# Kernel optimization log

Measured on AMD Instinct MI355X. Metric: run time of the kernel, lower is better.

The kernel has to match this reference:

```python
import jax, jax.numpy as jnp
import numpy as np

DIM = 1024
NHEAD = 16
HEAD_DIM = DIM // NHEAD
B, S, L = 1, 4096, 4096


def setup_inputs() -> dict:
    key = jax.random.key(0)
    ks = jax.random.split(key, 11)
    scale = 1.0 / np.sqrt(DIM)
    inp = {
        'query': jax.random.normal(ks[0], (B, S, DIM), dtype=jnp.float32),
        'key': jax.random.normal(ks[1], (B, L, DIM), dtype=jnp.float32),
        'value': jax.random.normal(ks[2], (B, L, DIM), dtype=jnp.float32),
        # torch nn.Linear weights: y = x @ W.T + b, W shape (out, in) = (DIM, DIM)
        'Wq': jax.random.normal(ks[3], (DIM, DIM), dtype=jnp.float32) * scale,
        'bq': jax.random.normal(ks[4], (DIM,), dtype=jnp.float32) * 0.01,
        'Wk': jax.random.normal(ks[5], (DIM, DIM), dtype=jnp.float32) * scale,
        'bk': jax.random.normal(ks[6], (DIM,), dtype=jnp.float32) * 0.01,
        'Wv': jax.random.normal(ks[7], (DIM, DIM), dtype=jnp.float32) * scale,
        'bv': jax.random.normal(ks[8], (DIM,), dtype=jnp.float32) * 0.01,
        'Wo': jax.random.normal(ks[9], (DIM, DIM), dtype=jnp.float32) * scale,
        'bo': jax.random.normal(ks[10], (DIM,), dtype=jnp.float32) * 0.01,
    }
    return inp


def _split_heads(x):
    # (B, T, D) -> (B, H, T, hd)
    b, t, _ = x.shape
    return x.reshape(b, t, NHEAD, HEAD_DIM).transpose(0, 2, 1, 3)


def reference(query, key, value, Wq, bq, Wk, bk, Wv, bv, Wo, bo):
    q = _split_heads(query @ Wq.T + bq)   # (B,H,S,hd)
    k = _split_heads(key @ Wk.T + bk)     # (B,H,L,hd)
    v = _split_heads(value @ Wv.T + bv)   # (B,H,L,hd)
    inv_sqrt_d = 1.0 / np.sqrt(HEAD_DIM).astype(np.float32)
    scores = jnp.einsum('bhsd,bhld->bhsl', q, k) * inv_sqrt_d
    probs = jax.nn.softmax(scores, axis=-1)
    ctx = jnp.einsum('bhsl,bhld->bhsd', probs, v)
    ctx = ctx.transpose(0, 2, 1, 3).reshape(query.shape[0], -1, DIM)
    return ctx @ Wo.T + bo
```

## Files before the change

kernel.cpp:

```cpp
#include <hip/hip_runtime.h>
#include <hip/hip_bf16.h>

#define DIM 1024
#define NHEAD 16
#define HD 64
#define SEQ 4096

typedef unsigned short u16;
typedef unsigned int u32;
typedef __attribute__((ext_vector_type(8))) short bf16x8;
typedef __attribute__((ext_vector_type(4))) float f32x4;
typedef __attribute__((ext_vector_type(16))) float f32x16;

__device__ __forceinline__ u16 f2bf(float x) {
  __hip_bfloat16 h = __float2bfloat16(x);
  return *reinterpret_cast<u16*>(&h);
}

__device__ __forceinline__ float bf2f(u16 u) {
  union { u32 u; float f; } c;
  c.u = ((u32)u) << 16;
  return c.f;
}

__device__ __forceinline__ float fexp2(float x) {
#if __has_builtin(__builtin_amdgcn_exp2f)
  return __builtin_amdgcn_exp2f(x);
#else
  return __expf(x * 0.69314718056f);
#endif
}

__device__ __forceinline__ u32 cvtpk(float a, float b) {
  u32 r;
  asm("v_cvt_pk_bf16_f32 %0, %1, %2" : "=v"(r) : "v"(a), "v"(b));
  return r;
}

__device__ __forceinline__ void pswap(u32& a, u32& b) {
  asm("v_permlane32_swap_b32 %0, %1" : "+v"(a), "+v"(b));
}

__device__ __forceinline__ void gload16(const u16* g, const u16* l) {
  __builtin_amdgcn_global_load_lds(
      (const __attribute__((address_space(1))) void*)g,
      (__attribute__((address_space(3))) void*)l, 16, 0, 0);
}

__global__ __launch_bounds__(256) void cvt_all(
    const float* __restrict__ q, const float* __restrict__ k, const float* __restrict__ v,
    const float* __restrict__ wq, const float* __restrict__ wk, const float* __restrict__ wv,
    const float* __restrict__ wo,
    u16* __restrict__ oq, u16* __restrict__ ok, u16* __restrict__ ov,
    u16* __restrict__ owq, u16* __restrict__ owk, u16* __restrict__ owv, u16* __restrict__ owo) {
  int b = blockIdx.x;
  const float* in;
  u16* out;
  int i;
  if (b < 12288) {
    int s = b >> 12;
    in = (s == 0) ? q : (s == 1) ? k : v;
    out = (s == 0) ? oq : (s == 1) ? ok : ov;
    i = (b & 4095) * 256 + threadIdx.x;
  } else {
    int bb = b - 12288;
    int s = bb >> 10;
    in = (s == 0) ? wq : (s == 1) ? wk : (s == 2) ? wv : wo;
    out = (s == 0) ? owq : (s == 1) ? owk : (s == 2) ? owv : owo;
    i = (bb & 1023) * 256 + threadIdx.x;
  }
  float4 val = ((const float4*)in)[i];
  ushort4 o;
  o.x = f2bf(val.x); o.y = f2bf(val.y); o.z = f2bf(val.z); o.w = f2bf(val.w);
  ((ushort4*)out)[i] = o;
}

__global__ __launch_bounds__(256, 3) void gemm_proj(
    const u16* __restrict__ qx, const u16* __restrict__ kx, const u16* __restrict__ vx,
    const u16* __restrict__ wqp, const u16* __restrict__ wkp, const u16* __restrict__ wvp,
    const float* __restrict__ bq, const float* __restrict__ bk, const float* __restrict__ bv,
    u16* __restrict__ Qb, u16* __restrict__ Kb, u16* __restrict__ Vt) {
  __shared__ u16 As[128][64];
  __shared__ u16 Bs[128][64];
  const int z = blockIdx.y;
  const u16 *Ag, *Bg;
  const float* bias;
  u16* outp;
  int mb, nb;
  float scale = 1.f;
  if (z == 0) {
    Ag = qx; Bg = wqp; bias = bq; outp = Qb;
    mb = blockIdx.x >> 3; nb = blockIdx.x & 7; scale = 0.18033688f;
  } else if (z == 1) {
    Ag = kx; Bg = wkp; bias = bk; outp = Kb;
    mb = blockIdx.x >> 3; nb = blockIdx.x & 7;
  } else {
    Ag = wvp; Bg = vx; bias = bv; outp = Vt;
    mb = blockIdx.x >> 5; nb = blockIdx.x & 31;
  }

  const int tid = threadIdx.x, lane = tid & 63, wid = tid >> 6;
  const int lq = lane & 15, g = lane >> 4;
  const int wr = wid >> 1, wc = wid & 1;
  const int m0 = mb * 128, n0 = nb * 128;
  const int sr = lane >> 3, ss = lane & 7;

  const u16* pA = Ag + (size_t)(m0 + wid * 32 + sr) * DIM + ((ss ^ sr) * 8);
  const u16* pB = Bg + (size_t)(n0 + wid * 32 + sr) * DIM + ((ss ^ sr) * 8);

  const f32x4 zero4 = {0.f, 0.f, 0.f, 0.f};
  f32x4 acc[4][4];
#pragma unroll
  for (int mi = 0; mi < 4; ++mi)
#pragma unroll
    for (int ni = 0; ni < 4; ++ni) acc[mi][ni] = zero4;

  for (int k0 = 0; k0 < DIM; k0 += 64) {
    __syncthreads();
#pragma unroll
    for (int i = 0; i < 4; ++i) {
      gload16(pA + i * 8 * DIM + k0, &As[wid * 32 + i * 8][0]);
      gload16(pB + i * 8 * DIM + k0, &Bs[wid * 32 + i * 8][0]);
    }
    __syncthreads();
#pragma unroll
    for (int kk = 0; kk < 2; ++kk) {
      bf16x8 a[4], b[4];
#pragma unroll
      for (int t4 = 0; t4 < 4; ++t4) {
        u32 offA = (u32)(wr * 64 + t4 * 16 + lq) * 128 + (u32)(((kk * 4 + g) ^ (lq & 7)) * 16);
        u32 offB = (u32)(wc * 64 + t4 * 16 + lq) * 128 + (u32)(((kk * 4 + g) ^ (lq & 7)) * 16);
        a[t4] = *(const bf16x8*)((const char*)As + offA);
        b[t4] = *(const bf16x8*)((const char*)Bs + offB);
      }
#pragma unroll
      for (int mi = 0; mi < 4; ++mi)
#pragma unroll
        for (int ni = 0; ni < 4; ++ni)
          acc[mi][ni] = __builtin_amdgcn_mfma_f32_16x16x32_bf16(a[mi], b[ni], acc[mi][ni], 0, 0, 0);
    }
  }

  if (z < 2) {
    float bn[4];
#pragma unroll
    for (int ni = 0; ni < 4; ++ni) bn[ni] = bias[n0 + wc * 64 + ni * 16 + lq];
#pragma unroll
    for (int mi = 0; mi < 4; ++mi)
#pragma unroll
      for (int r = 0; r < 4; ++r) {
        int mm = m0 + wr * 64 + mi * 16 + g * 4 + r;
#pragma unroll
        for (int ni = 0; ni < 4; ++ni) {
          int nn = n0 + wc * 64 + ni * 16 + lq;
          float v = (acc[mi][ni][r] + bn[ni]) * scale;
          outp[((size_t)(nn >> 6) * SEQ + mm) * 64 + (nn & 63)] = f2bf(v);
        }
      }
  } else {
#pragma unroll
    for (int mi = 0; mi < 4; ++mi)
#pragma unroll
      for (int r = 0; r < 4; ++r) {
        int mm = m0 + wr * 64 + mi * 16 + g * 4 + r;
        float bm = bias[mm];
#pragma unroll
        for (int ni = 0; ni < 4; ++ni) {
          int nn = n0 + wc * 64 + ni * 16 + lq;
          outp[(size_t)mm * SEQ + nn] = f2bf(acc[mi][ni][r] + bm);
        }
      }
  }
}

__global__ __launch_bounds__(256) void gemm_out(
    const u16* __restrict__ Ag, const u16* __restrict__ Bg,
    const float* __restrict__ bias, float* __restrict__ outp) {
  __shared__ u16 As[128][64];
  __shared__ u16 Bs[128][64];
  const int tid = threadIdx.x, lane = tid & 63, wid = tid >> 6;
  const int lq = lane & 15, g = lane >> 4;
  const int wr = wid >> 1, wc = wid & 1;
  const int m0 = blockIdx.x * 128, n0 = blockIdx.y * 128;
  const int sr = lane >> 3, ss = lane & 7;

  const u16* pA = Ag + (size_t)(m0 + wid * 32 + sr) * DIM + ((ss ^ sr) * 8);
  const u16* pB = Bg + (size_t)(n0 + wid * 32 + sr) * DIM + ((ss ^ sr) * 8);

  const f32x4 zero4 = {0.f, 0.f, 0.f, 0.f};
  f32x4 acc[4][4];
#pragma unroll
  for (int mi = 0; mi < 4; ++mi)
#pragma unroll
    for (int ni = 0; ni < 4; ++ni) acc[mi][ni] = zero4;

  for (int k0 = 0; k0 < DIM; k0 += 64) {
    __syncthreads();
#pragma unroll
    for (int i = 0; i < 4; ++i) {
      gload16(pA + i * 8 * DIM + k0, &As[wid * 32 + i * 8][0]);
      gload16(pB + i * 8 * DIM + k0, &Bs[wid * 32 + i * 8][0]);
    }
    __syncthreads();
#pragma unroll
    for (int kk = 0; kk < 2; ++kk) {
      bf16x8 a[4], b[4];
#pragma unroll
      for (int t4 = 0; t4 < 4; ++t4) {
        u32 offA = (u32)(wr * 64 + t4 * 16 + lq) * 128 + (u32)(((kk * 4 + g) ^ (lq & 7)) * 16);
        u32 offB = (u32)(wc * 64 + t4 * 16 + lq) * 128 + (u32)(((kk * 4 + g) ^ (lq & 7)) * 16);
        a[t4] = *(const bf16x8*)((const char*)As + offA);
        b[t4] = *(const bf16x8*)((const char*)Bs + offB);
      }
#pragma unroll
      for (int mi = 0; mi < 4; ++mi)
#pragma unroll
        for (int ni = 0; ni < 4; ++ni)
          acc[mi][ni] = __builtin_amdgcn_mfma_f32_16x16x32_bf16(a[mi], b[ni], acc[mi][ni], 0, 0, 0);
    }
  }

  float bn[4];
#pragma unroll
  for (int ni = 0; ni < 4; ++ni) bn[ni] = bias[n0 + wc * 64 + ni * 16 + lq];
#pragma unroll
  for (int mi = 0; mi < 4; ++mi)
#pragma unroll
    for (int r = 0; r < 4; ++r) {
      int mm = m0 + wr * 64 + mi * 16 + g * 4 + r;
#pragma unroll
      for (int ni = 0; ni < 4; ++ni) {
        int nn = n0 + wc * 64 + ni * 16 + lq;
        outp[(size_t)mm * DIM + nn] = acc[mi][ni][r] + bn[ni];
      }
    }
}

__global__ __launch_bounds__(256, 2) void attn32(
    const u16* __restrict__ Qb, const u16* __restrict__ Kb,
    const u16* __restrict__ Vtb, u16* __restrict__ po,
    float* __restrict__ pl) {
  __shared__ u16 Ks[2][64][64];
  __shared__ u16 Vs[2][64][64];
  const int tid = threadIdx.x, lane = tid & 63, wid = tid >> 6;
  const int q5 = lane & 31, hi = lane >> 5;
  const int bid = blockIdx.x;
  const int rest = bid >> 3;
  const int h = (bid & 7) * 2 + (rest >> 6);
  const int kv = (rest >> 5) & 1;
  const int qbase = (rest & 31) * 128 + wid * 32;

  const u16* Qg = Qb + (size_t)h * SEQ * HD;
  const u16* Kg = Kb + (size_t)h * SEQ * HD;
  const u16* Vg = Vtb + (size_t)h * HD * SEQ;

  const int sr = lane >> 3, ss = lane & 7;
  const u16* pK = Kg + (size_t)(kv * 2048 + wid * 16 + sr) * HD + ((ss ^ sr) * 8);
  const u16* pV = Vg + (size_t)(wid * 16 + sr) * SEQ + kv * 2048 + ((ss ^ sr) * 8);

  u32 roff[8];
#pragma unroll
  for (int ks = 0; ks < 4; ++ks) {
    u32 slot = (u32)((ks * 2 + hi) ^ (q5 & 7));
    roff[ks * 2] = (u32)q5 * 128 + slot * 16;
    roff[ks * 2 + 1] = (u32)(32 + q5) * 128 + slot * 16;
  }
  const char* KsB = (const char*)Ks;
  const char* VsB = (const char*)Vs;

  bf16x8 qf[4];
#pragma unroll
  for (int ks = 0; ks < 4; ++ks)
    qf[ks] = *(const bf16x8*)(Qg + (size_t)(qbase + q5) * HD + ks * 16 + hi * 8);

  bf16x8 ones;
#pragma unroll
  for (int j = 0; j < 8; ++j) ones[j] = (short)0x3F80;

  f32x16 o0, o1, osum, zv;
#pragma unroll
  for (int j = 0; j < 16; ++j) { o0[j] = 0.f; o1[j] = 0.f; osum[j] = 0.f; zv[j] = 0.f; }

  gload16(pK, &Ks[0][wid * 16][0]);
  gload16(pK + 8 * HD, &Ks[0][wid * 16 + 8][0]);
  gload16(pV, &Vs[0][wid * 16][0]);
  gload16(pV + 8 * SEQ, &Vs[0][wid * 16 + 8][0]);
  const u16* pKn = pK + 64 * HD;
  const u16* pVn = pV + 64;
  __syncthreads();

  const int NT = 2048 / 64;

#define ATTN_BODY(CB, PF)                                                     \
  {                                                                           \
    if (PF) {                                                                 \
      gload16(pKn, &Ks[(CB) ^ 1][wid * 16][0]);                               \
      gload16(pKn + 8 * HD, &Ks[(CB) ^ 1][wid * 16 + 8][0]);                  \
      gload16(pVn, &Vs[(CB) ^ 1][wid * 16][0]);                               \
      gload16(pVn + 8 * SEQ, &Vs[(CB) ^ 1][wid * 16 + 8][0]);                 \
      pKn += 64 * HD;                                                         \
      pVn += 64;                                                              \
    }                                                                         \
    f32x16 s0, s1;                                                            \
    __builtin_amdgcn_s_setprio(1);                                            \
    {                                                                         \
      bf16x8 ka0 = *(const bf16x8*)(KsB + (CB) * 8192 + roff[0]);             \
      bf16x8 ka1 = *(const bf16x8*)(KsB + (CB) * 8192 + roff[1]);             \
      s0 = __builtin_amdgcn_mfma_f32_32x32x16_bf16(ka0, qf[0], zv, 0, 0, 0);  \
      s1 = __builtin_amdgcn_mfma_f32_32x32x16_bf16(ka1, qf[0], zv, 0, 0, 0);  \
    }                                                                         \
    _Pragma("unroll")                                                         \
    for (int ks = 1; ks < 4; ++ks) {                                          \
      bf16x8 ka0 = *(const bf16x8*)(KsB + (CB) * 8192 + roff[ks * 2]);        \
      bf16x8 ka1 = *(const bf16x8*)(KsB + (CB) * 8192 + roff[ks * 2 + 1]);    \
      s0 = __builtin_amdgcn_mfma_f32_32x32x16_bf16(ka0, qf[ks], s0, 0, 0, 0); \
      s1 = __builtin_amdgcn_mfma_f32_32x32x16_bf16(ka1, qf[ks], s1, 0, 0, 0); \
    }                                                                         \
    __builtin_amdgcn_s_setprio(0);                                            \
    _Pragma("unroll")                                                         \
    for (int j = 0; j < 16; ++j) s0[j] = fexp2(s0[j]);                        \
    _Pragma("unroll")                                                         \
    for (int j = 0; j < 16; ++j) s1[j] = fexp2(s1[j]);                        \
    u32 pk0[8], pk1[8];                                                       \
    _Pragma("unroll")                                                         \
    for (int i2 = 0; i2 < 8; ++i2) {                                          \
      pk0[i2] = cvtpk(s0[2 * i2], s0[2 * i2 + 1]);                            \
      pk1[i2] = cvtpk(s1[2 * i2], s1[2 * i2 + 1]);                            \
    }                                                                         \
    bf16x8 W[4];                                                              \
    _Pragma("unroll")                                                         \
    for (int kss = 0; kss < 2; ++kss) {                                       \
      {                                                                       \
        u32 a = pk0[4 * kss], b = pk0[4 * kss + 2];                           \
        u32 c = pk0[4 * kss + 1], d = pk0[4 * kss + 3];                       \
        pswap(a, b);                                                          \
        pswap(c, d);                                                          \
        union { u32 u[4]; bf16x8 v; } tt;                                     \
        tt.u[0] = a; tt.u[1] = c; tt.u[2] = b; tt.u[3] = d;                   \
        W[kss] = tt.v;                                                        \
      }                                                                       \
      {                                                                       \
        u32 a = pk1[4 * kss], b = pk1[4 * kss + 2];                           \
        u32 c = pk1[4 * kss + 1], d = pk1[4 * kss + 3];                       \
        pswap(a, b);                                                          \
        pswap(c, d);                                                          \
        union { u32 u[4]; bf16x8 v; } tt;                                     \
        tt.u[0] = a; tt.u[1] = c; tt.u[2] = b; tt.u[3] = d;                   \
        W[2 + kss] = tt.v;                                                    \
      }                                                                       \
    }                                                                         \
    __builtin_amdgcn_s_setprio(1);                                            \
    _Pragma("unroll")                                                         \
    for (int ks = 0; ks < 4; ++ks) {                                          \
      bf16x8 va0 = *(const bf16x8*)(VsB + (CB) * 8192 + roff[ks * 2]);        \
      bf16x8 va1 = *(const bf16x8*)(VsB + (CB) * 8192 + roff[ks * 2 + 1]);    \
      o0 = __builtin_amdgcn_mfma_f32_32x32x16_bf16(va0, W[ks], o0, 0, 0, 0);  \
      o1 = __builtin_amdgcn_mfma_f32_32x32x16_bf16(va1, W[ks], o1, 0, 0, 0);  \
      osum = __builtin_amdgcn_mfma_f32_32x32x16_bf16(ones, W[ks], osum, 0, 0, 0); \
    }                                                                         \
    __builtin_amdgcn_s_setprio(0);                                            \
    __syncthreads();                                                          \
  }

  for (int t = 0; t < NT; t += 2) {
    ATTN_BODY(0, true);
    ATTN_BODY(1, (t + 2 < NT));
  }
#undef ATTN_BODY

  float lsum = osum[0];
  float inv = 1.f / lsum;
  size_t ridx = (size_t)(kv * 16 + h) * 4096 + qbase + q5;
  u16* cp = po + ridx * 64;
#pragma unroll
  for (int rg = 0; rg < 4; ++rg) {
    ushort4 pa, pb;
    pa.x = f2bf(o0[rg * 4 + 0] * inv); pa.y = f2bf(o0[rg * 4 + 1] * inv);
    pa.z = f2bf(o0[rg * 4 + 2] * inv); pa.w = f2bf(o0[rg * 4 + 3] * inv);
    pb.x = f2bf(o1[rg * 4 + 0] * inv); pb.y = f2bf(o1[rg * 4 + 1] * inv);
    pb.z = f2bf(o1[rg * 4 + 2] * inv); pb.w = f2bf(o1[rg * 4 + 3] * inv);
    *(ushort4*)(cp + rg * 8 + 4 * hi) = pa;
    *(ushort4*)(cp + 32 + rg * 8 + 4 * hi) = pb;
  }
  if (hi == 0) pl[ridx] = lsum;
}

__global__ __launch_bounds__(256) void combine(
    const u16* __restrict__ po, const float* __restrict__ pl,
    u16* __restrict__ cx) {
  const int tid = threadIdx.x;
  const int R = blockIdx.x * 64 + (tid >> 2);
  const int h = R >> 12, q = R & 4095;
  const int dbase = (tid & 3) * 16;
  const int idx0 = R;
  const int idx1 = R + 16 * 4096;
  float l0 = pl[idx0], l1 = pl[idx1];
  float inv = 1.f / (l0 + l1);
  float a0 = l0 * inv, a1 = l1 * inv;
  const u16* p0 = po + (size_t)idx0 * 64 + dbase;
  const u16* p1 = po + (size_t)idx1 * 64 + dbase;
  u16* cp = cx + (size_t)q * DIM + h * 64 + dbase;
#pragma unroll
  for (int v = 0; v < 2; ++v) {
    bf16x8 x0 = *(const bf16x8*)(p0 + v * 8);
    bf16x8 x1 = *(const bf16x8*)(p1 + v * 8);
    union { u16 u[8]; bf16x8 v8; } r;
#pragma unroll
    for (int j = 0; j < 8; ++j)
      r.u[j] = f2bf(a0 * bf2f((u16)x0[j]) + a1 * bf2f((u16)x1[j]));
    *(bf16x8*)(cp + v * 8) = r.v8;
  }
}

extern "C" void kernel_launch(void* const* d_in, const int* in_sizes, int n_in,
                              void* d_out, int out_size, void* d_ws, size_t ws_size,
                              hipStream_t stream) {
  const float* query = (const float*)d_in[0];
  const float* key_  = (const float*)d_in[1];
  const float* value = (const float*)d_in[2];
  const float* Wq = (const float*)d_in[3]; const float* bq = (const float*)d_in[4];
  const float* Wk = (const float*)d_in[5]; const float* bk = (const float*)d_in[6];
  const float* Wv = (const float*)d_in[7]; const float* bv = (const float*)d_in[8];
  const float* Wo = (const float*)d_in[9]; const float* bo = (const float*)d_in[10];

  char* ws = (char*)d_ws;
  const size_t MB = 1024 * 1024;
  u16* qx = (u16*)(ws);
  u16* kx = (u16*)(ws + 8 * MB);
  u16* vx = (u16*)(ws + 16 * MB);
  u16* wq = (u16*)(ws + 24 * MB);
  u16* wk = (u16*)(ws + 26 * MB);
  u16* wv = (u16*)(ws + 28 * MB);
  u16* wo = (u16*)(ws + 30 * MB);
  u16* Qb = (u16*)(ws + 32 * MB);
  u16* Kb = (u16*)(ws + 40 * MB);
  u16* Vt = (u16*)(ws + 48 * MB);
  u16* cx = (u16*)(ws + 56 * MB);
  u16* po = (u16*)(ws);
  float* pl = (float*)(ws + 16 * MB);

  cvt_all<<<dim3(16384), 256, 0, stream>>>(query, key_, value, Wq, Wk, Wv, Wo,
                                           qx, kx, vx, wq, wk, wv, wo);

  gemm_proj<<<dim3(256, 3), 256, 0, stream>>>(qx, kx, vx, wq, wk, wv,
                                              bq, bk, bv, Qb, Kb, Vt);

  attn32<<<dim3(1024), 256, 0, stream>>>(Qb, Kb, Vt, po, pl);

  combine<<<dim3(1024), 256, 0, stream>>>(po, pl, cx);

  gemm_out<<<dim3(32, 8), 256, 0, stream>>>(cx, wo, bo, (float*)d_out);
}
```

Measured before the change: 169.8 us.

## Process two 32-row query tiles per wave and compute row sums with VALU

Each wave now handles 64 query rows (two 32-row tiles) instead of 32, so every K/V fragment read from LDS feeds twice as many MFMAs, and the grid is halved. The extra MFMA against a ones vector that produced the softmax denominator is replaced by a VALU sum of the exponentiated scores plus a cross-half shuffle. This cuts LDS traffic per FLOP and MFMA work, but doubles accumulator and score register usage, which may hurt occupancy under the 2-blocks launch bound, and leaves only 512 blocks to spread over the CUs.

```diff
diff --git a/kernel.cpp b/kernel.cpp
--- a/kernel.cpp
+++ b/kernel.cpp
@@ -45,6 +45,15 @@
   __builtin_amdgcn_global_load_lds(
       (const __attribute__((address_space(1))) void*)g,
       (__attribute__((address_space(3))) void*)l, 16, 0, 0);
+}
+
+__device__ __forceinline__ float vsum16(const f32x16& v) {
+  float a[8];
+#pragma unroll
+  for (int j = 0; j < 8; ++j) a[j] = v[j] + v[j + 8];
+#pragma unroll
+  for (int j = 0; j < 4; ++j) a[j] = a[j] + a[j + 4];
+  return (a[0] + a[2]) + (a[1] + a[3]);
 }
 
 __global__ __launch_bounds__(256) void cvt_all(
@@ -246,9 +255,9 @@
   const int q5 = lane & 31, hi = lane >> 5;
   const int bid = blockIdx.x;
   const int rest = bid >> 3;
-  const int h = (bid & 7) * 2 + (rest >> 6);
-  const int kv = (rest >> 5) & 1;
-  const int qbase = (rest & 31) * 128 + wid * 32;
+  const int h = (bid & 7) * 2 + (rest >> 5);
+  const int kv = (rest >> 4) & 1;
+  const int qbase = (rest & 15) * 256 + wid * 64;
 
   const u16* Qg = Qb + (size_t)h * SEQ * HD;
   const u16* Kg = Kb + (size_t)h * SEQ * HD;
@@ -268,18 +277,19 @@
   const char* KsB = (const char*)Ks;
   const char* VsB = (const char*)Vs;
 
-  bf16x8 qf[4];
-#pragma unroll
-  for (int ks = 0; ks < 4; ++ks)
-    qf[ks] = *(const bf16x8*)(Qg + (size_t)(qbase + q5) * HD + ks * 16 + hi * 8);
-
-  bf16x8 ones;
-#pragma unroll
-  for (int j = 0; j < 8; ++j) ones[j] = (short)0x3F80;
-
-  f32x16 o0, o1, osum, zv;
-#pragma unroll
-  for (int j = 0; j < 16; ++j) { o0[j] = 0.f; o1[j] = 0.f; osum[j] = 0.f; zv[j] = 0.f; }
+  bf16x8 qfA[4], qfB[4];
+#pragma unroll
+  for (int ks = 0; ks < 4; ++ks) {
+    qfA[ks] = *(const bf16x8*)(Qg + (size_t)(qbase + q5) * HD + ks * 16 + hi * 8);
+    qfB[ks] = *(const bf16x8*)(Qg + (size_t)(qbase + 32 + q5) * HD + ks * 16 + hi * 8);
+  }
+
+  f32x16 oA0, oA1, oB0, oB1, zv;
+#pragma unroll
+  for (int j = 0; j < 16; ++j) {
+    oA0[j] = 0.f; oA1[j] = 0.f; oB0[j] = 0.f; oB1[j] = 0.f; zv[j] = 0.f;
+  }
+  float lsumA = 0.f, lsumB = 0.f;
 
   gload16(pK, &Ks[0][wid * 16][0]);
   gload16(pK + 8 * HD, &Ks[0][wid * 16 + 8][0]);
@@ -291,75 +301,92 @@
 
   const int NT = 2048 / 64;
 
-#define ATTN_BODY(CB, PF)                                                     \
-  {                                                                           \
-    if (PF) {                                                                 \
-      gload16(pKn, &Ks[(CB) ^ 1][wid * 16][0]);                               \
-      gload16(pKn + 8 * HD, &Ks[(CB) ^ 1][wid * 16 + 8][0]);                  \
-      gload16(pVn, &Vs[(CB) ^ 1][wid * 16][0]);                               \
-      gload16(pVn + 8 * SEQ, &Vs[(CB) ^ 1][wid * 16 + 8][0]);                 \
-      pKn += 64 * HD;                                                         \
-      pVn += 64;                                                              \
+#define PACK_W(W, pk0, pk1)                                                   \
+  _Pragma("unroll")                                                           \
+  for (int kss = 0; kss < 2; ++kss) {                                         \
+    {                                                                         \
+      u32 a = pk0[4 * kss], b = pk0[4 * kss + 2];                             \
+      u32 c = pk0[4 * kss + 1], d = pk0[4 * kss + 3];                         \
+      pswap(a, b);                                                            \
+      pswap(c, d);                                                            \
+      union { u32 u[4]; bf16x8 v; } tt;                                       \
+      tt.u[0] = a; tt.u[1] = c; tt.u[2] = b; tt.u[3] = d;                     \
+      W[kss] = tt.v;                                                          \
     }                                                                         \
-    f32x16 s0, s1;                                                            \
-    __builtin_amdgcn_s_setprio(1);                                            \
     {                                                                         \
-      bf16x8 ka0 = *(const bf16x8*)(KsB + (CB) * 8192 + roff[0]);             \
-      bf16x8 ka1 = *(const bf16x8*)(KsB + (CB) * 8192 + roff[1]);             \
-      s0 = __builtin_amdgcn_mfma_f32_32x32x16_bf16(ka0, qf[0], zv, 0, 0, 0);  \
-      s1 = __builtin_amdgcn_mfma_f32_32x32x16_bf16(ka1, qf[0], zv, 0, 0, 0);  \
+      u32 a = pk1[4 * kss], b = pk1[4 * kss + 2];                             \
+      u32 c = pk1[4 * kss + 1], d = pk1[4 * kss + 3];                         \
+      pswap(a, b);                                                            \
+      pswap(c, d);                                                            \
+      union { u32 u[4]; bf16x8 v; } tt;                                       \
+      tt.u[0] = a; tt.u[1] = c; tt.u[2] = b; tt.u[3] = d;                     \
+      W[2 + kss] = tt.v;                                                      \
     }                                                                         \
-    _Pragma("unroll")                                                         \
-    for (int ks = 1; ks < 4; ++ks) {                                          \
-      bf16x8 ka0 = *(const bf16x8*)(KsB + (CB) * 8192 + roff[ks * 2]);        \
-      bf16x8 ka1 = *(const bf16x8*)(KsB + (CB) * 8192 + roff[ks * 2 + 1]);    \
-      s0 = __builtin_amdgcn_mfma_f32_32x32x16_bf16(ka0, qf[ks], s0, 0, 0, 0); \
-      s1 = __builtin_amdgcn_mfma_f32_32x32x16_bf16(ka1, qf[ks], s1, 0, 0, 0); \
-    }                                                                         \
-    __builtin_amdgcn_s_setprio(0);                                            \
-    _Pragma("unroll")                                                         \
-    for (int j = 0; j < 16; ++j) s0[j] = fexp2(s0[j]);                        \
-    _Pragma("unroll")                                                         \
-    for (int j = 0; j < 16; ++j) s1[j] = fexp2(s1[j]);                        \
-    u32 pk0[8], pk1[8];                                                       \
-    _Pragma("unroll")                                                         \
-    for (int i2 = 0; i2 < 8; ++i2) {                                          \
-      pk0[i2] = cvtpk(s0[2 * i2], s0[2 * i2 + 1]);                            \
-      pk1[i2] = cvtpk(s1[2 * i2], s1[2 * i2 + 1]);                            \
-    }                                                                         \
-    bf16x8 W[4];                                                              \
-    _Pragma("unroll")                                                         \
-    for (int kss = 0; kss < 2; ++kss) {                                       \
-      {                                                                       \
-        u32 a = pk0[4 * kss], b = pk0[4 * kss + 2];                           \
-        u32 c = pk0[4 * kss + 1], d = pk0[4 * kss + 3];                       \
-        pswap(a, b);                                                          \
-        pswap(c, d);                                                          \
-        union { u32 u[4]; bf16x8 v; } tt;                                     \
-        tt.u[0] = a; tt.u[1] = c; tt.u[2] = b; tt.u[3] = d;                   \
-        W[kss] = tt.v;                                                        \
-      }                                                                       \
-      {                                                                       \
-        u32 a = pk1[4 * kss], b = pk1[4 * kss + 2];                           \
-        u32 c = pk1[4 * kss + 1], d = pk1[4 * kss + 3];                       \
-        pswap(a, b);                                                          \
-        pswap(c, d);                                                          \
-        union { u32 u[4]; bf16x8 v; } tt;                                     \
-        tt.u[0] = a; tt.u[1] = c; tt.u[2] = b; tt.u[3] = d;                   \
-        W[2 + kss] = tt.v;                                                    \
-      }                                                                       \
-    }                                                                         \
-    __builtin_amdgcn_s_setprio(1);                                            \
-    _Pragma("unroll")                                                         \
-    for (int ks = 0; ks < 4; ++ks) {                                          \
-      bf16x8 va0 = *(const bf16x8*)(VsB + (CB) * 8192 + roff[ks * 2]);        \
-      bf16x8 va1 = *(const bf16x8*)(VsB + (CB) * 8192 + roff[ks * 2 + 1]);    \
-      o0 = __builtin_amdgcn_mfma_f32_32x32x16_bf16(va0, W[ks], o0, 0, 0, 0);  \
-      o1 = __builtin_amdgcn_mfma_f32_32x32x16_bf16(va1, W[ks], o1, 0, 0, 0);  \
-      osum = __builtin_amdgcn_mfma_f32_32x32x16_bf16(ones, W[ks], osum, 0, 0, 0); \
-    }                                                                         \
-    __builtin_amdgcn_s_setprio(0);                                            \
-    __syncthreads();                                                          \
+  }
+
+#define ATTN_BODY(CB, PF)                                                       \
+  {                                                                             \
+    if (PF) {                                                                   \
+      gload16(pKn, &Ks[(CB) ^ 1][wid * 16][0]);                                 \
+      gload16(pKn + 8 * HD, &Ks[(CB) ^ 1][wid * 16 + 8][0]);                    \
+      gload16(pVn, &Vs[(CB) ^ 1][wid * 16][0]);                                 \
+      gload16(pVn + 8 * SEQ, &Vs[(CB) ^ 1][wid * 16 + 8][0]);                   \
+      pKn += 64 * HD;                                                           \
+      pVn += 64;                                                                \
+    }                                                                           \
+    f32x16 sA0, sA1, sB0, sB1;                                                  \
+    __builtin_amdgcn_s_setprio(1);                                              \
+    {                                                                           \
+      bf16x8 ka0 = *(const bf16x8*)(KsB + (CB) * 8192 + roff[0]);               \
+      bf16x8 ka1 = *(const bf16x8*)(KsB + (CB) * 8192 + roff[1]);               \
+      sA0 = __builtin_amdgcn_mfma_f32_32x32x16_bf16(ka0, qfA[0], zv, 0, 0, 0);  \
+      sA1 = __builtin_amdgcn_mfma_f32_32x32x16_bf16(ka1, qfA[0], zv, 0, 0, 0);  \
+      sB0 = __builtin_amdgcn_mfma_f32_32x32x16_bf16(ka0, qfB[0], zv, 0, 0, 0);  \
+      sB1 = __builtin_amdgcn_mfma_f32_32x32x16_bf16(ka1, qfB[0], zv, 0, 0, 0);  \
+    }                                                                           \
+    _Pragma("unroll")                                                           \
+    for (int ks = 1; ks < 4; ++ks) {                                            \
+      bf16x8 ka0 = *(const bf16x8*)(KsB + (CB) * 8192 + roff[ks * 2]);          \
+      bf16x8 ka1 = *(const bf16x8*)(KsB + (CB) * 8192 + roff[ks * 2 + 1]);      \
+      sA0 = __builtin_amdgcn_mfma_f32_32x32x16_bf16(ka0, qfA[ks], sA0, 0, 0, 0);\
+      sA1 = __builtin_amdgcn_mfma_f32_32x32x16_bf16(ka1, qfA[ks], sA1, 0, 0, 0);\
+      sB0 = __builtin_amdgcn_mfma_f32_32x32x16_bf16(ka0, qfB[ks], sB0, 0, 0, 0);\
+      sB1 = __builtin_amdgcn_mfma_f32_32x32x16_bf16(ka1, qfB[ks], sB1, 0, 0, 0);\
+    }                                                                           \
+    __builtin_amdgcn_s_setprio(0);                                              \
+    _Pragma("unroll")                                                           \
+    for (int j = 0; j < 16; ++j) sA0[j] = fexp2(sA0[j]);                        \
+    _Pragma("unroll")                                                           \
+    for (int j = 0; j < 16; ++j) sA1[j] = fexp2(sA1[j]);                        \
+    _Pragma("unroll")                                                           \
+    for (int j = 0; j < 16; ++j) sB0[j] = fexp2(sB0[j]);                        \
+    _Pragma("unroll")                                                           \
+    for (int j = 0; j < 16; ++j) sB1[j] = fexp2(sB1[j]);                        \
+    lsumA += vsum16(sA0) + vsum16(sA1);                                         \
+    lsumB += vsum16(sB0) + vsum16(sB1);                                         \
+    u32 pkA0[8], pkA1[8], pkB0[8], pkB1[8];                                     \
+    _Pragma("unroll")                                                           \
+    for (int i2 = 0; i2 < 8; ++i2) {                                            \
+      pkA0[i2] = cvtpk(sA0[2 * i2], sA0[2 * i2 + 1]);                           \
+      pkA1[i2] = cvtpk(sA1[2 * i2], sA1[2 * i2 + 1]);                           \
+      pkB0[i2] = cvtpk(sB0[2 * i2], sB0[2 * i2 + 1]);                           \
+      pkB1[i2] = cvtpk(sB1[2 * i2], sB1[2 * i2 + 1]);                           \
+    }                                                                           \
+    bf16x8 WA[4], WB[4];                                                        \
+    PACK_W(WA, pkA0, pkA1)                                                      \
+    PACK_W(WB, pkB0, pkB1)                                                      \
+    __builtin_amdgcn_s_setprio(1);                                              \
+    _Pragma("unroll")                                                           \
+    for (int ks = 0; ks < 4; ++ks) {                                            \
+      bf16x8 va0 = *(const bf16x8*)(VsB + (CB) * 8192 + roff[ks * 2]);          \
+      bf16x8 va1 = *(const bf16x8*)(VsB + (CB) * 8192 + roff[ks * 2 + 1]);      \
+      oA0 = __builtin_amdgcn_mfma_f32_32x32x16_bf16(va0, WA[ks], oA0, 0, 0, 0); \
+      oA1 = __builtin_amdgcn_mfma_f32_32x32x16_bf16(va1, WA[ks], oA1, 0, 0, 0); \
+      oB0 = __builtin_amdgcn_mfma_f32_32x32x16_bf16(va0, WB[ks], oB0, 0, 0, 0); \
+      oB1 = __builtin_amdgcn_mfma_f32_32x32x16_bf16(va1, WB[ks], oB1, 0, 0, 0); \
+    }                                                                           \
+    __builtin_amdgcn_s_setprio(0);                                              \
+    __syncthreads();                                                            \
   }
 
   for (int t = 0; t < NT; t += 2) {
@@ -367,22 +394,36 @@
     ATTN_BODY(1, (t + 2 < NT));
   }
 #undef ATTN_BODY
-
-  float lsum = osum[0];
-  float inv = 1.f / lsum;
-  size_t ridx = (size_t)(kv * 16 + h) * 4096 + qbase + q5;
-  u16* cp = po + ridx * 64;
+#undef PACK_W
+
+  lsumA += __shfl_xor(lsumA, 32);
+  lsumB += __shfl_xor(lsumB, 32);
+  float invA = 1.f / lsumA;
+  float invB = 1.f / lsumB;
+  size_t ridxA = (size_t)(kv * 16 + h) * 4096 + qbase + q5;
+  size_t ridxB = ridxA + 32;
+  u16* cpA = po + ridxA * 64;
+  u16* cpB = po + ridxB * 64;
 #pragma unroll
   for (int rg = 0; rg < 4; ++rg) {
     ushort4 pa, pb;
-    pa.x = f2bf(o0[rg * 4 + 0] * inv); pa.y = f2bf(o0[rg * 4 + 1] * inv);
-    pa.z = f2bf(o0[rg * 4 + 2] * inv); pa.w = f2bf(o0[rg * 4 + 3] * inv);
-    pb.x = f2bf(o1[rg * 4 + 0] * inv); pb.y = f2bf(o1[rg * 4 + 1] * inv);
-    pb.z = f2bf(o1[rg * 4 + 2] * inv); pb.w = f2bf(o1[rg * 4 + 3] * inv);
-    *(ushort4*)(cp + rg * 8 + 4 * hi) = pa;
-    *(ushort4*)(cp + 32 + rg * 8 + 4 * hi) = pb;
-  }
-  if (hi == 0) pl[ridx] = lsum;
+    pa.x = f2bf(oA0[rg * 4 + 0] * invA); pa.y = f2bf(oA0[rg * 4 + 1] * invA);
+    pa.z = f2bf(oA0[rg * 4 + 2] * invA); pa.w = f2bf(oA0[rg * 4 + 3] * invA);
+    pb.x = f2bf(oA1[rg * 4 + 0] * invA); pb.y = f2bf(oA1[rg * 4 + 1] * invA);
+    pb.z = f2bf(oA1[rg * 4 + 2] * invA); pb.w = f2bf(oA1[rg * 4 + 3] * invA);
+    *(ushort4*)(cpA + rg * 8 + 4 * hi) = pa;
+    *(ushort4*)(cpA + 32 + rg * 8 + 4 * hi) = pb;
+    pa.x = f2bf(oB0[rg * 4 + 0] * invB); pa.y = f2bf(oB0[rg * 4 + 1] * invB);
+    pa.z = f2bf(oB0[rg * 4 + 2] * invB); pa.w = f2bf(oB0[rg * 4 + 3] * invB);
+    pb.x = f2bf(oB1[rg * 4 + 0] * invB); pb.y = f2bf(oB1[rg * 4 + 1] * invB);
+    pb.z = f2bf(oB1[rg * 4 + 2] * invB); pb.w = f2bf(oB1[rg * 4 + 3] * invB);
+    *(ushort4*)(cpB + rg * 8 + 4 * hi) = pa;
+    *(ushort4*)(cpB + 32 + rg * 8 + 4 * hi) = pb;
+  }
+  if (hi == 0) {
+    pl[ridxA] = lsumA;
+    pl[ridxB] = lsumB;
+  }
 }
 
 __global__ __launch_bounds__(256) void combine(
@@ -445,7 +486,7 @@
   gemm_proj<<<dim3(256, 3), 256, 0, stream>>>(qx, kx, vx, wq, wk, wv,
                                               bq, bk, bv, Qb, Kb, Vt);
 
-  attn32<<<dim3(1024), 256, 0, stream>>>(Qb, Kb, Vt, po, pl);
+  attn32<<<dim3(512), 256, 0, stream>>>(Qb, Kb, Vt, po, pl);
 
   combine<<<dim3(1024), 256, 0, stream>>>(po, pl, cx);
 
```

Result: faster. 156.4 us (-7.9%).

## Split attention KV into four chunks, drop MFMA row-sum, shrink output GEMM tile

Applied to the files above, without the earlier changes.

Attention now splits the 4096-key range into four chunks instead of two, doubling the grid to 2048 blocks and raising the occupancy hint to 4. The combine kernel merges four partial outputs. The softmax denominator is now summed in VALU with a cross-half shuffle instead of an extra ones-matrix MFMA per step, which removes a third of the PV-stage MFMA work. The output GEMM uses 64x128 tiles with a 2-block occupancy hint, giving 512 blocks instead of 256 to fill more CUs. In exchange, the extra partials add global traffic and combine work, and the workspace layout is reshuffled.

```diff
diff --git a/kernel.cpp b/kernel.cpp
--- a/kernel.cpp
+++ b/kernel.cpp
@@ -45,6 +45,15 @@
   __builtin_amdgcn_global_load_lds(
       (const __attribute__((address_space(1))) void*)g,
       (__attribute__((address_space(3))) void*)l, 16, 0, 0);
+}
+
+__device__ __forceinline__ float vsum16(const f32x16& v) {
+  float a[8];
+#pragma unroll
+  for (int j = 0; j < 8; ++j) a[j] = v[j] + v[j + 8];
+#pragma unroll
+  for (int j = 0; j < 4; ++j) a[j] = a[j] + a[j + 4];
+  return (a[0] + a[2]) + (a[1] + a[3]);
 }
 
 __global__ __launch_bounds__(256) void cvt_all(
@@ -173,47 +182,51 @@
   }
 }
 
-__global__ __launch_bounds__(256) void gemm_out(
+__global__ __launch_bounds__(256, 2) void gemm_out(
     const u16* __restrict__ Ag, const u16* __restrict__ Bg,
     const float* __restrict__ bias, float* __restrict__ outp) {
-  __shared__ u16 As[128][64];
+  __shared__ u16 As[64][64];
   __shared__ u16 Bs[128][64];
   const int tid = threadIdx.x, lane = tid & 63, wid = tid >> 6;
   const int lq = lane & 15, g = lane >> 4;
   const int wr = wid >> 1, wc = wid & 1;
-  const int m0 = blockIdx.x * 128, n0 = blockIdx.y * 128;
+  const int m0 = blockIdx.x * 64, n0 = blockIdx.y * 128;
   const int sr = lane >> 3, ss = lane & 7;
 
-  const u16* pA = Ag + (size_t)(m0 + wid * 32 + sr) * DIM + ((ss ^ sr) * 8);
+  const u16* pA = Ag + (size_t)(m0 + wid * 16 + sr) * DIM + ((ss ^ sr) * 8);
   const u16* pB = Bg + (size_t)(n0 + wid * 32 + sr) * DIM + ((ss ^ sr) * 8);
 
   const f32x4 zero4 = {0.f, 0.f, 0.f, 0.f};
-  f32x4 acc[4][4];
-#pragma unroll
-  for (int mi = 0; mi < 4; ++mi)
+  f32x4 acc[2][4];
+#pragma unroll
+  for (int mi = 0; mi < 2; ++mi)
 #pragma unroll
     for (int ni = 0; ni < 4; ++ni) acc[mi][ni] = zero4;
 
   for (int k0 = 0; k0 < DIM; k0 += 64) {
     __syncthreads();
 #pragma unroll
-    for (int i = 0; i < 4; ++i) {
-      gload16(pA + i * 8 * DIM + k0, &As[wid * 32 + i * 8][0]);
+    for (int i = 0; i < 2; ++i)
+      gload16(pA + i * 8 * DIM + k0, &As[wid * 16 + i * 8][0]);
+#pragma unroll
+    for (int i = 0; i < 4; ++i)
       gload16(pB + i * 8 * DIM + k0, &Bs[wid * 32 + i * 8][0]);
-    }
     __syncthreads();
 #pragma unroll
     for (int kk = 0; kk < 2; ++kk) {
-      bf16x8 a[4], b[4];
+      bf16x8 a[2], b[4];
+#pragma unroll
+      for (int t4 = 0; t4 < 2; ++t4) {
+        u32 offA = (u32)(wr * 32 + t4 * 16 + lq) * 128 + (u32)(((kk * 4 + g) ^ (lq & 7)) * 16);
+        a[t4] = *(const bf16x8*)((const char*)As + offA);
+      }
 #pragma unroll
       for (int t4 = 0; t4 < 4; ++t4) {
-        u32 offA = (u32)(wr * 64 + t4 * 16 + lq) * 128 + (u32)(((kk * 4 + g) ^ (lq & 7)) * 16);
         u32 offB = (u32)(wc * 64 + t4 * 16 + lq) * 128 + (u32)(((kk * 4 + g) ^ (lq & 7)) * 16);
-        a[t4] = *(const bf16x8*)((const char*)As + offA);
         b[t4] = *(const bf16x8*)((const char*)Bs + offB);
       }
 #pragma unroll
-      for (int mi = 0; mi < 4; ++mi)
+      for (int mi = 0; mi < 2; ++mi)
 #pragma unroll
         for (int ni = 0; ni < 4; ++ni)
           acc[mi][ni] = __builtin_amdgcn_mfma_f32_16x16x32_bf16(a[mi], b[ni], acc[mi][ni], 0, 0, 0);
@@ -224,10 +237,10 @@
 #pragma unroll
   for (int ni = 0; ni < 4; ++ni) bn[ni] = bias[n0 + wc * 64 + ni * 16 + lq];
 #pragma unroll
-  for (int mi = 0; mi < 4; ++mi)
+  for (int mi = 0; mi < 2; ++mi)
 #pragma unroll
     for (int r = 0; r < 4; ++r) {
-      int mm = m0 + wr * 64 + mi * 16 + g * 4 + r;
+      int mm = m0 + wr * 32 + mi * 16 + g * 4 + r;
 #pragma unroll
       for (int ni = 0; ni < 4; ++ni) {
         int nn = n0 + wc * 64 + ni * 16 + lq;
@@ -236,18 +249,18 @@
     }
 }
 
-__global__ __launch_bounds__(256, 2) void attn32(
+__global__ __launch_bounds__(256, 4) void attn32(
     const u16* __restrict__ Qb, const u16* __restrict__ Kb,
-    const u16* __restrict__ Vtb, u16* __restrict__ po,
-    float* __restrict__ pl) {
+    const u16* __restrict__ Vtb, u16* __restrict__ poA,
+    u16* __restrict__ poB, float* __restrict__ pl) {
   __shared__ u16 Ks[2][64][64];
   __shared__ u16 Vs[2][64][64];
   const int tid = threadIdx.x, lane = tid & 63, wid = tid >> 6;
   const int q5 = lane & 31, hi = lane >> 5;
   const int bid = blockIdx.x;
   const int rest = bid >> 3;
-  const int h = (bid & 7) * 2 + (rest >> 6);
-  const int kv = (rest >> 5) & 1;
+  const int h = (bid & 7) * 2 + (rest >> 7);
+  const int kv = (rest >> 5) & 3;
   const int qbase = (rest & 31) * 128 + wid * 32;
 
   const u16* Qg = Qb + (size_t)h * SEQ * HD;
@@ -255,8 +268,8 @@
   const u16* Vg = Vtb + (size_t)h * HD * SEQ;
 
   const int sr = lane >> 3, ss = lane & 7;
-  const u16* pK = Kg + (size_t)(kv * 2048 + wid * 16 + sr) * HD + ((ss ^ sr) * 8);
-  const u16* pV = Vg + (size_t)(wid * 16 + sr) * SEQ + kv * 2048 + ((ss ^ sr) * 8);
+  const u16* pK = Kg + (size_t)(kv * 1024 + wid * 16 + sr) * HD + ((ss ^ sr) * 8);
+  const u16* pV = Vg + (size_t)(wid * 16 + sr) * SEQ + kv * 1024 + ((ss ^ sr) * 8);
 
   u32 roff[8];
 #pragma unroll
@@ -273,13 +286,10 @@
   for (int ks = 0; ks < 4; ++ks)
     qf[ks] = *(const bf16x8*)(Qg + (size_t)(qbase + q5) * HD + ks * 16 + hi * 8);
 
-  bf16x8 ones;
-#pragma unroll
-  for (int j = 0; j < 8; ++j) ones[j] = (short)0x3F80;
-
-  f32x16 o0, o1, osum, zv;
-#pragma unroll
-  for (int j = 0; j < 16; ++j) { o0[j] = 0.f; o1[j] = 0.f; osum[j] = 0.f; zv[j] = 0.f; }
+  f32x16 o0, o1, zv;
+#pragma unroll
+  for (int j = 0; j < 16; ++j) { o0[j] = 0.f; o1[j] = 0.f; zv[j] = 0.f; }
+  float lsum = 0.f;
 
   gload16(pK, &Ks[0][wid * 16][0]);
   gload16(pK + 8 * HD, &Ks[0][wid * 16 + 8][0]);
@@ -289,7 +299,30 @@
   const u16* pVn = pV + 64;
   __syncthreads();
 
-  const int NT = 2048 / 64;
+  const int NT = 1024 / 64;
+
+#define PACK_W(W, pk0, pk1)                                                   \
+  _Pragma("unroll")                                                           \
+  for (int kss = 0; kss < 2; ++kss) {                                         \
+    {                                                                         \
+      u32 a = pk0[4 * kss], b = pk0[4 * kss + 2];                             \
+      u32 c = pk0[4 * kss + 1], d = pk0[4 * kss + 3];                         \
+      pswap(a, b);                                                            \
+      pswap(c, d);                                                            \
+      union { u32 u[4]; bf16x8 v; } tt;                                       \
+      tt.u[0] = a; tt.u[1] = c; tt.u[2] = b; tt.u[3] = d;                     \
+      W[kss] = tt.v;                                                          \
+    }                                                                         \
+    {                                                                         \
+      u32 a = pk1[4 * kss], b = pk1[4 * kss + 2];                             \
+      u32 c = pk1[4 * kss + 1], d = pk1[4 * kss + 3];                         \
+      pswap(a, b);                                                            \
+      pswap(c, d);                                                            \
+      union { u32 u[4]; bf16x8 v; } tt;                                       \
+      tt.u[0] = a; tt.u[1] = c; tt.u[2] = b; tt.u[3] = d;                     \
+      W[2 + kss] = tt.v;                                                      \
+    }                                                                         \
+  }
 
 #define ATTN_BODY(CB, PF)                                                     \
   {                                                                           \
@@ -321,6 +354,7 @@
     for (int j = 0; j < 16; ++j) s0[j] = fexp2(s0[j]);                        \
     _Pragma("unroll")                                                         \
     for (int j = 0; j < 16; ++j) s1[j] = fexp2(s1[j]);                        \
+    lsum += vsum16(s0) + vsum16(s1);                                          \
     u32 pk0[8], pk1[8];                                                       \
     _Pragma("unroll")                                                         \
     for (int i2 = 0; i2 < 8; ++i2) {                                          \
@@ -328,27 +362,7 @@
       pk1[i2] = cvtpk(s1[2 * i2], s1[2 * i2 + 1]);                            \
     }                                                                         \
     bf16x8 W[4];                                                              \
-    _Pragma("unroll")                                                         \
-    for (int kss = 0; kss < 2; ++kss) {                                       \
-      {                                                                       \
-        u32 a = pk0[4 * kss], b = pk0[4 * kss + 2];                           \
-        u32 c = pk0[4 * kss + 1], d = pk0[4 * kss + 3];                       \
-        pswap(a, b);                                                          \
-        pswap(c, d);                                                          \
-        union { u32 u[4]; bf16x8 v; } tt;                                     \
-        tt.u[0] = a; tt.u[1] = c; tt.u[2] = b; tt.u[3] = d;                   \
-        W[kss] = tt.v;                                                        \
-      }                                                                       \
-      {                                                                       \
-        u32 a = pk1[4 * kss], b = pk1[4 * kss + 2];                           \
-        u32 c = pk1[4 * kss + 1], d = pk1[4 * kss + 3];                       \
-        pswap(a, b);                                                          \
-        pswap(c, d);                                                          \
-        union { u32 u[4]; bf16x8 v; } tt;                                     \
-        tt.u[0] = a; tt.u[1] = c; tt.u[2] = b; tt.u[3] = d;                   \
-        W[2 + kss] = tt.v;                                                    \
-      }                                                                       \
-    }                                                                         \
+    PACK_W(W, pk0, pk1)                                                       \
     __builtin_amdgcn_s_setprio(1);                                            \
     _Pragma("unroll")                                                         \
     for (int ks = 0; ks < 4; ++ks) {                                          \
@@ -356,7 +370,6 @@
       bf16x8 va1 = *(const bf16x8*)(VsB + (CB) * 8192 + roff[ks * 2 + 1]);    \
       o0 = __builtin_amdgcn_mfma_f32_32x32x16_bf16(va0, W[ks], o0, 0, 0, 0);  \
       o1 = __builtin_amdgcn_mfma_f32_32x32x16_bf16(va1, W[ks], o1, 0, 0, 0);  \
-      osum = __builtin_amdgcn_mfma_f32_32x32x16_bf16(ones, W[ks], osum, 0, 0, 0); \
     }                                                                         \
     __builtin_amdgcn_s_setprio(0);                                            \
     __syncthreads();                                                          \
@@ -367,11 +380,14 @@
     ATTN_BODY(1, (t + 2 < NT));
   }
 #undef ATTN_BODY
-
-  float lsum = osum[0];
+#undef PACK_W
+
+  lsum += __shfl_xor(lsum, 32);
   float inv = 1.f / lsum;
-  size_t ridx = (size_t)(kv * 16 + h) * 4096 + qbase + q5;
-  u16* cp = po + ridx * 64;
+  const size_t PO_STRIDE = (size_t)16 * 4096 * 64;
+  u16* pob = (kv < 3) ? (poA + (size_t)kv * PO_STRIDE) : poB;
+  size_t rA = (size_t)h * 4096 + qbase + q5;
+  u16* cp = pob + rA * 64;
 #pragma unroll
   for (int rg = 0; rg < 4; ++rg) {
     ushort4 pa, pb;
@@ -382,32 +398,39 @@
     *(ushort4*)(cp + rg * 8 + 4 * hi) = pa;
     *(ushort4*)(cp + 32 + rg * 8 + 4 * hi) = pb;
   }
-  if (hi == 0) pl[ridx] = lsum;
+  if (hi == 0) pl[(size_t)(kv * 16 + h) * 4096 + qbase + q5] = lsum;
 }
 
 __global__ __launch_bounds__(256) void combine(
-    const u16* __restrict__ po, const float* __restrict__ pl,
-    u16* __restrict__ cx) {
+    const u16* __restrict__ poA, const u16* __restrict__ poB,
+    const float* __restrict__ pl, u16* __restrict__ cx) {
   const int tid = threadIdx.x;
   const int R = blockIdx.x * 64 + (tid >> 2);
   const int h = R >> 12, q = R & 4095;
   const int dbase = (tid & 3) * 16;
-  const int idx0 = R;
-  const int idx1 = R + 16 * 4096;
-  float l0 = pl[idx0], l1 = pl[idx1];
-  float inv = 1.f / (l0 + l1);
-  float a0 = l0 * inv, a1 = l1 * inv;
-  const u16* p0 = po + (size_t)idx0 * 64 + dbase;
-  const u16* p1 = po + (size_t)idx1 * 64 + dbase;
+  const size_t PO_STRIDE = (size_t)16 * 4096 * 64;
+  float l0 = pl[R];
+  float l1 = pl[R + 65536];
+  float l2 = pl[R + 2 * 65536];
+  float l3 = pl[R + 3 * 65536];
+  float inv = 1.f / (l0 + l1 + l2 + l3);
+  float a0 = l0 * inv, a1 = l1 * inv, a2 = l2 * inv, a3 = l3 * inv;
+  const u16* p0 = poA + (size_t)R * 64 + dbase;
+  const u16* p1 = p0 + PO_STRIDE;
+  const u16* p2 = p1 + PO_STRIDE;
+  const u16* p3 = poB + (size_t)R * 64 + dbase;
   u16* cp = cx + (size_t)q * DIM + h * 64 + dbase;
 #pragma unroll
   for (int v = 0; v < 2; ++v) {
     bf16x8 x0 = *(const bf16x8*)(p0 + v * 8);
     bf16x8 x1 = *(const bf16x8*)(p1 + v * 8);
+    bf16x8 x2 = *(const bf16x8*)(p2 + v * 8);
+    bf16x8 x3 = *(const bf16x8*)(p3 + v * 8);
     union { u16 u[8]; bf16x8 v8; } r;
 #pragma unroll
     for (int j = 0; j < 8; ++j)
-      r.u[j] = f2bf(a0 * bf2f((u16)x0[j]) + a1 * bf2f((u16)x1[j]));
+      r.u[j] = f2bf(a0 * bf2f((u16)x0[j]) + a1 * bf2f((u16)x1[j]) +
+                    a2 * bf2f((u16)x2[j]) + a3 * bf2f((u16)x3[j]));
     *(bf16x8*)(cp + v * 8) = r.v8;
   }
 }
@@ -435,9 +458,10 @@
   u16* Qb = (u16*)(ws + 32 * MB);
   u16* Kb = (u16*)(ws + 40 * MB);
   u16* Vt = (u16*)(ws + 48 * MB);
-  u16* cx = (u16*)(ws + 56 * MB);
-  u16* po = (u16*)(ws);
-  float* pl = (float*)(ws + 16 * MB);
+  u16* poA = (u16*)(ws);
+  u16* poB = (u16*)(ws + 56 * MB);
+  float* pl = (float*)(ws + 24 * MB);
+  u16* cx = (u16*)(ws + 32 * MB);
 
   cvt_all<<<dim3(16384), 256, 0, stream>>>(query, key_, value, Wq, Wk, Wv, Wo,
                                            qx, kx, vx, wq, wk, wv, wo);
@@ -445,9 +469,9 @@
   gemm_proj<<<dim3(256, 3), 256, 0, stream>>>(qx, kx, vx, wq, wk, wv,
                                               bq, bk, bv, Qb, Kb, Vt);
 
-  attn32<<<dim3(1024), 256, 0, stream>>>(Qb, Kb, Vt, po, pl);
-
-  combine<<<dim3(1024), 256, 0, stream>>>(po, pl, cx);
-
-  gemm_out<<<dim3(32, 8), 256, 0, stream>>>(cx, wo, bo, (float*)d_out);
-}
+  attn32<<<dim3(2048), 256, 0, stream>>>(Qb, Kb, Vt, poA, poB, pl);
+
+  combine<<<dim3(1024), 256, 0, stream>>>(poA, poB, pl, cx);
+
+  gemm_out<<<dim3(64, 8), 256, 0, stream>>>(cx, wo, bo, (float*)d_out);
+}
```

Result: faster. 161.2 us (-5.1%).
